# Performance work log

Hardware: AMD Instinct MI355X
Metric: run time of the kernel (lower is better)

Reference implementation:

```python
import jax, jax.numpy as jnp
import numpy as np

L = 262144      # number of points
C = 256         # in_channels
NH = 8          # num_heads
G = 64          # group_size
FF = 2048       # torch TransformerEncoderLayer default dim_feedforward
LPAD = 262144   # padded length, divisible by G; LPAD//G divisible by batch_size
BS = 4


def setup_inputs() -> dict:
    key = jax.random.key(0)
    ks = jax.random.split(key, 12)
    def w(k, shape, scale=0.02):
        return jax.random.normal(k, shape, jnp.float32) * scale
    return {
        "feats_flat": jax.random.normal(ks[0], (L, C), jnp.float32),
        "x_idx": jax.random.randint(ks[1], (L,), 0, L),
        "flat2win": jax.random.randint(ks[2], (LPAD,), 0, L),
        "win2flat": jax.random.randint(ks[3], (L,), 0, LPAD),
        "in_proj_w": w(ks[4], (3 * C, C)),
        "in_proj_b": jnp.zeros((3 * C,), jnp.float32),
        "out_proj_w": w(ks[5], (C, C)),
        "out_proj_b": jnp.zeros((C,), jnp.float32),
        "lin1_w": w(ks[6], (FF, C)),
        "lin1_b": jnp.zeros((FF,), jnp.float32),
        "lin2_w": w(ks[7], (C, FF)),
        "lin2_b": jnp.zeros((C,), jnp.float32),
        "ln1_g": jnp.ones((C,), jnp.float32),
        "ln1_b": jnp.zeros((C,), jnp.float32),
        "ln2_g": jnp.ones((C,), jnp.float32),
        "ln2_b": jnp.zeros((C,), jnp.float32),
        "proj_w": w(ks[8], (C, 2 * C)),
        "proj_b": jnp.zeros((C,), jnp.float32),
        "batch_size": BS,
    }


def _layer_norm(x, g, b, eps=1e-5):
    mu = jnp.mean(x, axis=-1, keepdims=True)
    var = jnp.var(x, axis=-1, keepdims=True)
    return (x - mu) * jax.lax.rsqrt(var + eps) * g + b


def _mha(x, in_proj_w, in_proj_b, out_proj_w, out_proj_b):
    B, S, Cm = x.shape
    hd = Cm // NH
    qkv = x @ in_proj_w.T + in_proj_b                      # [B,S,3C]
    q, k, v = jnp.split(qkv, 3, axis=-1)
    q = q.reshape(B, S, NH, hd)
    k = k.reshape(B, S, NH, hd)
    v = v.reshape(B, S, NH, hd)
    scores = jnp.einsum("bqhd,bkhd->bhqk", q, k) / jnp.sqrt(jnp.float32(hd))
    attn = jax.nn.softmax(scores, axis=-1)
    out = jnp.einsum("bhqk,bkhd->bqhd", attn, v).reshape(B, S, Cm)
    return out @ out_proj_w.T + out_proj_b


def reference(feats_flat, x_idx, flat2win, win2flat,
              in_proj_w, in_proj_b, out_proj_w, out_proj_b,
              lin1_w, lin1_b, lin2_w, lin2_b,
              ln1_g, ln1_b, ln2_g, ln2_b,
              proj_w, proj_b, batch_size):
    Cc = feats_flat.shape[1]
    # gather: feats_flat[indices][flat2win] -> [NW, G, C]
    feats_win = feats_flat[x_idx][flat2win].reshape(-1, G, Cc)
    # adaptive max pool over the group axis -> [NW, C]
    feats_pool = jnp.max(feats_win, axis=1)
    # torch TransformerEncoderLayer (post-norm, relu, eval/no-dropout)
    x = feats_pool.reshape(batch_size, -1, Cc)             # [B, S, C]
    x = _layer_norm(x + _mha(x, in_proj_w, in_proj_b, out_proj_w, out_proj_b), ln1_g, ln1_b)
    ff = jax.nn.relu(x @ lin1_w.T + lin1_b) @ lin2_w.T + lin2_b
    x = _layer_norm(x + ff, ln2_g, ln2_b)
    feats_global = x.reshape(-1, Cc)                       # [NW, C]
    # broadcast global feature to every group element, concat (global first)
    fuse_in = jnp.concatenate(
        [jnp.broadcast_to(feats_global[:, None, :], feats_win.shape), feats_win],
        axis=-1)                                           # [NW, G, 2C]
    feats_fuse = (fuse_in @ proj_w.T + proj_b).reshape(-1, Cc)  # [LPAD, C]
    # scatter back: feats_flat[indices] = feats_fuse[win2flat]
    return feats_flat.at[x_idx].set(feats_fuse[win2flat])
```

## Files before the change

### kernel.cpp

```cpp
#include <hip/hip_runtime.h>
#include <math.h>

namespace {
constexpr int kL    = 262144;
constexpr int kC    = 256;
constexpr int kNH   = 8;
constexpr int kG    = 64;
constexpr int kFF   = 2048;
constexpr int kLPAD = 262144;
constexpr int kBS   = 4;
constexpr int kNW   = kLPAD / kG;
constexpr int kS    = kNW / kBS;
constexpr int kHD   = kC / kNH;

constexpr size_t MB        = 1024 * 1024;
constexpr size_t OFF_GIDX   = 0;
constexpr size_t OFF_WINNER = 1 * MB;
constexpr size_t OFF_WLIST  = 2 * MB;
constexpr size_t OFF_CNT    = 3 * MB;
constexpr size_t OFF_X0     = 4 * MB;
constexpr size_t OFF_BASE   = 8 * MB;
constexpr size_t OFF_ATTN   = 12 * MB;
constexpr size_t OFF_QH     = 16 * MB;
constexpr size_t OFF_KH     = 18 * MB;
constexpr size_t OFF_VH     = 20 * MB;
constexpr size_t OFF_X1     = 24 * MB;
constexpr size_t OFF_FF1    = 32 * MB;
constexpr size_t OFF_WINB   = 64 * MB;
constexpr size_t OFF_WOUTB  = OFF_WINB  + 512 * 1024;
constexpr size_t OFF_W1B    = OFF_WOUTB + 256 * 1024;
constexpr size_t OFF_W2B    = OFF_W1B   + 1536 * 1024;
constexpr size_t OFF_WP1B   = OFF_W2B   + 1536 * 1024;
constexpr size_t OFF_WP2B   = OFF_WP1B  + 256 * 1024;

typedef __attribute__((ext_vector_type(8))) short bf16x8;
typedef __attribute__((ext_vector_type(4))) float f32x4;

__device__ inline unsigned short f2bf(float f) {
  union { float f; unsigned int u; } x; x.f = f;
  unsigned int r = x.u + 0x7fff + ((x.u >> 16) & 1);
  return (unsigned short)(r >> 16);
}
}

__global__ __launch_bounds__(256) void k_initw(int* __restrict__ winner,
                                               int* __restrict__ cnt) {
  int i = blockIdx.x * 256 + threadIdx.x;
  ((int4*)winner)[i] = make_int4(-1, -1, -1, -1);
  if (i == 0) cnt[0] = 0;
}

__global__ __launch_bounds__(256) void k_winner(const int* __restrict__ x_idx,
                                                int* __restrict__ winner) {
  int i0 = (blockIdx.x * 256 + threadIdx.x) * 4;
  int4 xi = *(const int4*)&x_idx[i0];
  atomicMax(&winner[xi.x], i0);
  atomicMax(&winner[xi.y], i0 + 1);
  atomicMax(&winner[xi.z], i0 + 2);
  atomicMax(&winner[xi.w], i0 + 3);
}

__global__ __launch_bounds__(256) void k_fc(const int* __restrict__ x_idx,
                                            const int* __restrict__ winner,
                                            int* __restrict__ wlist,
                                            int* __restrict__ cnt,
                                            const float* __restrict__ in_proj_w,
                                            const float* __restrict__ out_proj_w,
                                            const float* __restrict__ lin1_w,
                                            const float* __restrict__ lin2_w,
                                            const float* __restrict__ proj_w,
                                            unsigned short* __restrict__ WINB,
                                            unsigned short* __restrict__ WOUTB,
                                            unsigned short* __restrict__ W1B,
                                            unsigned short* __restrict__ W2B,
                                            unsigned short* __restrict__ WP1,
                                            unsigned short* __restrict__ WP2) {
  int blk = blockIdx.x, t = threadIdx.x;
  if (blk < 256) {
    int i0 = (blk * 256 + t) * 4;
    int4 xi = *(const int4*)&x_idx[i0];
    #pragma unroll
    for (int j = 0; j < 4; ++j) {
      int i = i0 + j;
      int xv = (j == 0) ? xi.x : (j == 1) ? xi.y : (j == 2) ? xi.z : xi.w;
      if (winner[xv] == i) {
        int p = atomicAdd(cnt, 1);
        wlist[p] = i;
      }
    }
    return;
  }
  int b2 = blk - 256;
  const float* src = nullptr; unsigned short* dst = nullptr; int i = 0;
  if (b2 < 192)       { src = in_proj_w;  dst = WINB;  i = b2 * 256 + t; }
  else if (b2 < 256)  { src = out_proj_w; dst = WOUTB; i = (b2 - 192) * 256 + t; }
  else if (b2 < 768)  { src = lin1_w;     dst = W1B;   i = (b2 - 256) * 256 + t; }
  else if (b2 < 1280) { src = lin2_w;     dst = W2B;   i = (b2 - 768) * 256 + t; }
  else {
    int c = b2 - 1280;
    WP1[c * kC + t] = f2bf(proj_w[(size_t)c * (2 * kC) + t]);
    WP2[c * kC + t] = f2bf(proj_w[(size_t)c * (2 * kC) + kC + t]);
    return;
  }
  float4 v = ((const float4*)src)[i];
  ushort4 b;
  b.x = f2bf(v.x); b.y = f2bf(v.y); b.z = f2bf(v.z); b.w = f2bf(v.w);
  ((ushort4*)dst)[i] = b;
}

__global__ __launch_bounds__(256) void k_pc(const float* __restrict__ feats,
                                            const int* __restrict__ x_idx,
                                            const int* __restrict__ flat2win,
                                            const int* __restrict__ winner,
                                            int* __restrict__ gidx,
                                            float* __restrict__ x0,
                                            float* __restrict__ out) {
  int blk = blockIdx.x, t = threadIdx.x;
  int w = t >> 6, lane = t & 63;
  if (blk < kNW) {
    __shared__ int rows[kG];
    __shared__ __align__(16) float mred[4][kC];
    if (t < kG) {
      int g = x_idx[flat2win[blk * kG + t]];
      rows[t] = g;
      gidx[blk * kG + t] = g;
    }
    __syncthreads();
    float4 mx = make_float4(-INFINITY, -INFINITY, -INFINITY, -INFINITY);
    #pragma unroll
    for (int i = 0; i < 16; ++i) {
      int r = rows[w * 16 + i];
      float4 v = *(const float4*)&feats[(size_t)r * kC + lane * 4];
      mx.x = fmaxf(mx.x, v.x); mx.y = fmaxf(mx.y, v.y);
      mx.z = fmaxf(mx.z, v.z); mx.w = fmaxf(mx.w, v.w);
    }
    *(float4*)&mred[w][lane * 4] = mx;
    __syncthreads();
    x0[blk * kC + t] = fmaxf(fmaxf(mred[0][t], mred[1][t]),
                             fmaxf(mred[2][t], mred[3][t]));
    return;
  }
  int cb = blk - kNW;
  #pragma unroll
  for (int i = 0; i < 2; ++i) {
    int row = cb * 8 + w * 2 + i;
    if (winner[row] < 0) {
      *(float4*)&out[(size_t)row * kC + lane * 4] =
          *(const float4*)&feats[(size_t)row * kC + lane * 4];
    }
  }
}

__global__ __launch_bounds__(256) void k_gemm_qkv(const float* __restrict__ A,
                                                  const unsigned short* __restrict__ Wb,
                                                  const float* __restrict__ bias,
                                                  unsigned short* __restrict__ Qh,
                                                  unsigned short* __restrict__ Kh,
                                                  unsigned short* __restrict__ Vh) {
  const float scale = 0.17677669529663687f;
  const int m0 = blockIdx.y * 64;
  const int sec = blockIdx.x;
  const int t = threadIdx.x;
  const int lane = t & 63, w = t >> 6;
  const int c0 = w * 64;
  const int kb = lane >> 4, lr = lane & 15;

  __shared__ __align__(16) unsigned short As[64 * 256];

  f32x4 acc[4][4] = {};
  #pragma unroll
  for (int i = 0; i < 16; ++i) {
    int row = i * 4 + w;
    float4 f4 = *(const float4*)&A[(size_t)(m0 + row) * kC + lane * 4];
    ushort4 b4;
    b4.x = f2bf(f4.x); b4.y = f2bf(f4.y); b4.z = f2bf(f4.z); b4.w = f2bf(f4.w);
    unsigned int off = (((unsigned)row * 512u) + (unsigned)lane * 8u) ^ (((unsigned)row & 7u) << 4);
    *(ushort4*)((char*)As + off) = b4;
  }
  __syncthreads();

  #pragma unroll
  for (int ks = 0; ks < 8; ++ks) {
    const int k0 = ks * 32;
    bf16x8 a[4], b[4];
    #pragma unroll
    for (int rt = 0; rt < 4; ++rt) {
      int row = rt * 16 + lr;
      unsigned int off = (((unsigned)row * 512u) + (unsigned)(k0 + kb * 8) * 2u) ^
                         (((unsigned)row & 7u) << 4);
      a[rt] = *(const bf16x8*)((const char*)As + off);
    }
    #pragma unroll
    for (int ct = 0; ct < 4; ++ct) {
      int c = sec * kC + c0 + ct * 16 + lr;
      b[ct] = *(const bf16x8*)&Wb[(size_t)c * kC + k0 + kb * 8];
    }
    #pragma unroll
    for (int rt = 0; rt < 4; ++rt)
      #pragma unroll
      for (int ct = 0; ct < 4; ++ct)
        acc[rt][ct] = __builtin_amdgcn_mfma_f32_16x16x32_bf16(a[rt], b[ct], acc[rt][ct], 0, 0, 0);
  }

  unsigned short* dstbuf = (sec == 0) ? Qh : (sec == 1) ? Kh : Vh;
  #pragma unroll
  for (int rt = 0; rt < 4; ++rt) {
    #pragma unroll
    for (int r = 0; r < 4; ++r) {
      int row = m0 + rt * 16 + kb * 4 + r;
      int bb = row >> 10, s = row & 1023;
      #pragma unroll
      for (int ct = 0; ct < 4; ++ct) {
        int c = c0 + ct * 16 + lr;
        float v = acc[rt][ct][r] + bias[sec * kC + c];
        if (sec == 0) v *= scale;
        int h = c >> 5, d = c & 31;
        dstbuf[(((size_t)(bb * kNH + h) * kS) + s) * kHD + d] = f2bf(v);
      }
    }
  }
}

__global__ __launch_bounds__(256) void k_attn(const unsigned short* __restrict__ Qh,
                                              const unsigned short* __restrict__ Kh,
                                              const unsigned short* __restrict__ Vh,
                                              unsigned short* __restrict__ attn_out) {
  const int q0 = blockIdx.x * 64;
  const int bh = blockIdx.y;
  const int b = bh >> 3, h = bh & 7;
  const int t = threadIdx.x;
  const int lane = t & 63, w = t >> 6;
  const int kb = lane >> 4, lr = lane & 15;

  __shared__ __align__(16) unsigned short Ks[128][40];
  __shared__ __align__(16) unsigned short VTs[32][136];
  __shared__ __align__(16) unsigned short Ps[4][16][136];

  bf16x8 aq = *(const bf16x8*)(Qh + (((size_t)bh * kS) + q0 + w * 16 + lr) * kHD + kb * 8);

  const unsigned short* kbase = Kh + (size_t)bh * kS * kHD;
  const unsigned short* vbase = Vh + (size_t)bh * kS * kHD;

  float m[4], l[4];
  f32x4 O[2] = {};
  #pragma unroll
  for (int r = 0; r < 4; ++r) { m[r] = -INFINITY; l[r] = 0.f; }

  for (int kt = 0; kt < kS / 128; ++kt) {
    {
      int key = t >> 1, d0 = (t & 1) * 16;
      size_t srow = ((size_t)(kt * 128 + key)) * kHD + d0;
      bf16x8 kv0 = *(const bf16x8*)(kbase + srow);
      bf16x8 kv1 = *(const bf16x8*)(kbase + srow + 8);
      *(bf16x8*)&Ks[key][d0] = kv0;
      *(bf16x8*)&Ks[key][d0 + 8] = kv1;
      bf16x8 vv0 = *(const bf16x8*)(vbase + srow);
      bf16x8 vv1 = *(const bf16x8*)(vbase + srow + 8);
      #pragma unroll
      for (int i = 0; i < 8; ++i) {
        VTs[d0 + i][key] = (unsigned short)vv0[i];
        VTs[d0 + 8 + i][key] = (unsigned short)vv1[i];
      }
    }
    __syncthreads();

    f32x4 S[8] = {};
    #pragma unroll
    for (int ct = 0; ct < 8; ++ct) {
      bf16x8 bk = *(const bf16x8*)&Ks[ct * 16 + lr][kb * 8];
      S[ct] = __builtin_amdgcn_mfma_f32_16x16x32_bf16(aq, bk, S[ct], 0, 0, 0);
    }

    float alpha[4];
    #pragma unroll
    for (int r = 0; r < 4; ++r) {
      float tmax = -INFINITY;
      #pragma unroll
      for (int ct = 0; ct < 8; ++ct) tmax = fmaxf(tmax, S[ct][r]);
      #pragma unroll
      for (int off = 8; off; off >>= 1) tmax = fmaxf(tmax, __shfl_xor(tmax, off, 16));
      float newm = fmaxf(m[r], tmax);
      alpha[r] = __expf(m[r] - newm);
      float ps = 0.f;
      #pragma unroll
      for (int ct = 0; ct < 8; ++ct) {
        float p = __expf(S[ct][r] - newm);
        ps += p;
        Ps[w][kb * 4 + r][ct * 16 + lr] = f2bf(p);
      }
      #pragma unroll
      for (int off = 8; off; off >>= 1) ps += __shfl_xor(ps, off, 16);
      l[r] = l[r] * alpha[r] + ps;
      m[r] = newm;
    }
    #pragma unroll
    for (int r = 0; r < 4; ++r) { O[0][r] *= alpha[r]; O[1][r] *= alpha[r]; }

    #pragma unroll
    for (int ks = 0; ks < 4; ++ks) {
      bf16x8 ap = *(const bf16x8*)&Ps[w][lr][ks * 32 + kb * 8];
      #pragma unroll
      for (int ct = 0; ct < 2; ++ct) {
        bf16x8 bv = *(const bf16x8*)&VTs[ct * 16 + lr][ks * 32 + kb * 8];
        O[ct] = __builtin_amdgcn_mfma_f32_16x16x32_bf16(ap, bv, O[ct], 0, 0, 0);
      }
    }
    __syncthreads();
  }

  #pragma unroll
  for (int ct = 0; ct < 2; ++ct) {
    #pragma unroll
    for (int r = 0; r < 4; ++r) {
      size_t row = (size_t)b * kS + q0 + w * 16 + kb * 4 + r;
      attn_out[row * kC + h * kHD + ct * 16 + lr] = f2bf(O[ct][r] / l[r]);
    }
  }
}

template <bool DO_BASE>
__global__ __launch_bounds__(256) void k_gemm_ln(const unsigned short* __restrict__ A,
                                                 int K,
                                                 const unsigned short* __restrict__ Wb,
                                                 const float* __restrict__ bias,
                                                 const float* __restrict__ R,
                                                 const float* __restrict__ g,
                                                 const float* __restrict__ bb,
                                                 float* __restrict__ Out,
                                                 const unsigned short* __restrict__ WbB,
                                                 const float* __restrict__ biasB) {
  const int m0 = blockIdx.x * 16;
  const int t = threadIdx.x;
  const int lane = t & 63, w = t >> 6;
  const int c0 = w * 64;
  const int kb = lane >> 4, lr = lane & 15;

  __shared__ __align__(16) unsigned short As[16 * 256];
  __shared__ __align__(16) unsigned short Xs[16 * 256];
  __shared__ float red[2][16][4];

  f32x4 acc[4] = {};
  for (int kc = 0; kc < K; kc += 256) {
    #pragma unroll
    for (int i = 0; i < 2; ++i) {
      int idx = i * 256 + t;
      int row = idx >> 5, seg = idx & 31;
      bf16x8 v = *(const bf16x8*)&A[(size_t)(m0 + row) * K + kc + seg * 8];
      unsigned int off = (((unsigned)row * 512u) + (unsigned)seg * 16u) ^ (((unsigned)row & 7u) << 4);
      *(bf16x8*)((char*)As + off) = v;
    }
    __syncthreads();

    #pragma unroll
    for (int ks = 0; ks < 8; ++ks) {
      const int k0 = ks * 32;
      unsigned int aoff = (((unsigned)lr * 512u) + (unsigned)(k0 + kb * 8) * 2u) ^
                          (((unsigned)lr & 7u) << 4);
      bf16x8 a = *(const bf16x8*)((const char*)As + aoff);
      #pragma unroll
      for (int ct = 0; ct < 4; ++ct) {
        bf16x8 b = *(const bf16x8*)&Wb[(size_t)(c0 + ct * 16 + lr) * K + kc + k0 + kb * 8];
        acc[ct] = __builtin_amdgcn_mfma_f32_16x16x32_bf16(a, b, acc[ct], 0, 0, 0);
      }
    }
    __syncthreads();
  }

  float v[4][4];
  float s[4], sq[4];
  #pragma unroll
  for (int r = 0; r < 4; ++r) { s[r] = 0.f; sq[r] = 0.f; }
  #pragma unroll
  for (int r = 0; r < 4; ++r) {
    int row = m0 + kb * 4 + r;
    #pragma unroll
    for (int ct = 0; ct < 4; ++ct) {
      int c = c0 + ct * 16 + lr;
      float x = acc[ct][r] + bias[c] + R[(size_t)row * kC + c];
      v[r][ct] = x;
      s[r] += x;
      sq[r] += x * x;
    }
  }
  #pragma unroll
  for (int r = 0; r < 4; ++r) {
    #pragma unroll
    for (int off = 8; off; off >>= 1) {
      s[r]  += __shfl_xor(s[r], off, 16);
      sq[r] += __shfl_xor(sq[r], off, 16);
    }
    if (lr == 0) { red[0][kb * 4 + r][w] = s[r]; red[1][kb * 4 + r][w] = sq[r]; }
  }
  __syncthreads();

  #pragma unroll
  for (int r = 0; r < 4; ++r) {
    int lrow = kb * 4 + r;
    float su = red[0][lrow][0] + red[0][lrow][1] + red[0][lrow][2] + red[0][lrow][3];
    float sg = red[1][lrow][0] + red[1][lrow][1] + red[1][lrow][2] + red[1][lrow][3];
    float mu = su * (1.0f / kC);
    float var = sg * (1.0f / kC) - mu * mu;
    float rs = rsqrtf(var + 1e-5f);
    #pragma unroll
    for (int ct = 0; ct < 4; ++ct) {
      int c = c0 + ct * 16 + lr;
      float yv = (v[r][ct] - mu) * rs * g[c] + bb[c];
      if (!DO_BASE) {
        Out[(size_t)(m0 + lrow) * kC + c] = yv;
      } else {
        unsigned int off = (((unsigned)lrow * 512u) + (unsigned)c * 2u) ^ (((unsigned)lrow & 7u) << 4);
        *(unsigned short*)((char*)Xs + off) = f2bf(yv);
      }
    }
  }

  if (DO_BASE) {
    __syncthreads();
    f32x4 acc2[4] = {};
    #pragma unroll
    for (int ks = 0; ks < 8; ++ks) {
      const int k0 = ks * 32;
      unsigned int aoff = (((unsigned)lr * 512u) + (unsigned)(k0 + kb * 8) * 2u) ^
                          (((unsigned)lr & 7u) << 4);
      bf16x8 a = *(const bf16x8*)((const char*)Xs + aoff);
      #pragma unroll
      for (int ct = 0; ct < 4; ++ct) {
        bf16x8 b = *(const bf16x8*)&WbB[(size_t)(c0 + ct * 16 + lr) * kC + k0 + kb * 8];
        acc2[ct] = __builtin_amdgcn_mfma_f32_16x16x32_bf16(a, b, acc2[ct], 0, 0, 0);
      }
    }
    #pragma unroll
    for (int r = 0; r < 4; ++r) {
      int row = m0 + kb * 4 + r;
      #pragma unroll
      for (int ct = 0; ct < 4; ++ct) {
        int c = c0 + ct * 16 + lr;
        Out[(size_t)row * kC + c] = acc2[ct][r] + biasB[c];
      }
    }
  }
}

__global__ __launch_bounds__(256) void k_gemm_ff1(const float* __restrict__ A,
                                                  const unsigned short* __restrict__ Wb,
                                                  const float* __restrict__ bias,
                                                  unsigned short* __restrict__ Cc) {
  const int m0 = blockIdx.y * 64;
  const int nb = blockIdx.x * 256;
  const int t = threadIdx.x;
  const int lane = t & 63, w = t >> 6;
  const int c0 = nb + w * 64;
  const int kb = lane >> 4, lr = lane & 15;

  __shared__ __align__(16) unsigned short As[64 * 256];

  f32x4 acc[4][4] = {};
  #pragma unroll
  for (int i = 0; i < 16; ++i) {
    int row = i * 4 + w;
    float4 f4 = *(const float4*)&A[(size_t)(m0 + row) * kC + lane * 4];
    ushort4 b4;
    b4.x = f2bf(f4.x); b4.y = f2bf(f4.y); b4.z = f2bf(f4.z); b4.w = f2bf(f4.w);
    unsigned int off = (((unsigned)row * 512u) + (unsigned)lane * 8u) ^ (((unsigned)row & 7u) << 4);
    *(ushort4*)((char*)As + off) = b4;
  }
  __syncthreads();

  #pragma unroll
  for (int ks = 0; ks < 8; ++ks) {
    const int k0 = ks * 32;
    bf16x8 a[4], b[4];
    #pragma unroll
    for (int rt = 0; rt < 4; ++rt) {
      int row = rt * 16 + lr;
      unsigned int off = (((unsigned)row * 512u) + (unsigned)(k0 + kb * 8) * 2u) ^
                         (((unsigned)row & 7u) << 4);
      a[rt] = *(const bf16x8*)((const char*)As + off);
    }
    #pragma unroll
    for (int ct = 0; ct < 4; ++ct) {
      int c = c0 + ct * 16 + lr;
      b[ct] = *(const bf16x8*)&Wb[(size_t)c * kC + k0 + kb * 8];
    }
    #pragma unroll
    for (int rt = 0; rt < 4; ++rt)
      #pragma unroll
      for (int ct = 0; ct < 4; ++ct)
        acc[rt][ct] = __builtin_amdgcn_mfma_f32_16x16x32_bf16(a[rt], b[ct], acc[rt][ct], 0, 0, 0);
  }

  #pragma unroll
  for (int rt = 0; rt < 4; ++rt) {
    #pragma unroll
    for (int r = 0; r < 4; ++r) {
      int row = m0 + rt * 16 + kb * 4 + r;
      #pragma unroll
      for (int ct = 0; ct < 4; ++ct) {
        int c = c0 + ct * 16 + lr;
        float vv = fmaxf(acc[rt][ct][r] + bias[c], 0.f);
        Cc[(size_t)row * kFF + c] = f2bf(vv);
      }
    }
  }
}

__global__ __launch_bounds__(256) void k_fuse(const float* __restrict__ feats,
                                              const int* __restrict__ gidx,
                                              const int* __restrict__ wlist,
                                              const int* __restrict__ cnt,
                                              const int* __restrict__ win2flat,
                                              const int* __restrict__ x_idx,
                                              const float* __restrict__ base,
                                              const unsigned short* __restrict__ W2B,
                                              float* __restrict__ out) {
  const int count = cnt[0];
  const int r0 = blockIdx.x * 64;
  if (r0 >= count) return;
  const int nr = min(64, count - r0);
  const int t = threadIdx.x;
  const int lane = t & 63, w = t >> 6;

  __shared__ __align__(16) unsigned short As[64 * 256];
  __shared__ int dstrow[64], wwin[64], srcrow[64];

  if (t < 64) {
    int rr = min(r0 + t, count - 1);
    int i = wlist[rr];
    int j = win2flat[i];
    srcrow[t] = gidx[j];
    wwin[t] = j >> 6;
    dstrow[t] = x_idx[i];
  }
  __syncthreads();

  for (int i = 0; i < 16; ++i) {
    int row = i * 4 + w;
    float4 f4 = *(const float4*)&feats[(size_t)srcrow[row] * kC + lane * 4];
    ushort4 b4;
    b4.x = f2bf(f4.x); b4.y = f2bf(f4.y); b4.z = f2bf(f4.z); b4.w = f2bf(f4.w);
    unsigned int off = (((unsigned)row * 512u) + (unsigned)lane * 8u) ^ (((unsigned)row & 7u) << 4);
    *(ushort4*)((char*)As + off) = b4;
  }
  __syncthreads();

  const int c0 = w * 64;
  const int kb = lane >> 4;
  const int lr = lane & 15;
  f32x4 acc[4][4] = {};
  for (int ks = 0; ks < 8; ++ks) {
    const int k0 = ks * 32;
    bf16x8 a[4], b[4];
    #pragma unroll
    for (int rt = 0; rt < 4; ++rt) {
      int row = rt * 16 + lr;
      unsigned int off = (((unsigned)row * 512u) + (unsigned)(k0 + kb * 8) * 2u) ^
                         (((unsigned)row & 7u) << 4);
      a[rt] = *(const bf16x8*)((const char*)As + off);
    }
    #pragma unroll
    for (int ct = 0; ct < 4; ++ct) {
      int c = c0 + ct * 16 + lr;
      b[ct] = *(const bf16x8*)&W2B[(size_t)c * kC + k0 + kb * 8];
    }
    #pragma unroll
    for (int rt = 0; rt < 4; ++rt)
      #pragma unroll
      for (int ct = 0; ct < 4; ++ct)
        acc[rt][ct] = __builtin_amdgcn_mfma_f32_16x16x32_bf16(a[rt], b[ct], acc[rt][ct], 0, 0, 0);
  }

  #pragma unroll
  for (int rt = 0; rt < 4; ++rt) {
    #pragma unroll
    for (int r = 0; r < 4; ++r) {
      int row = rt * 16 + kb * 4 + r;
      if (row < nr) {
        size_t orow = (size_t)dstrow[row] * kC;
        size_t brow = (size_t)wwin[row] * kC;
        #pragma unroll
        for (int ct = 0; ct < 4; ++ct) {
          int c = c0 + ct * 16 + lr;
          out[orow + c] = acc[rt][ct][r] + base[brow + c];
        }
      }
    }
  }
}

extern "C" void kernel_launch(void* const* d_in, const int* in_sizes, int n_in,
                              void* d_out, int out_size, void* d_ws, size_t ws_size,
                              hipStream_t stream) {
  const float* feats      = (const float*)d_in[0];
  const int*   x_idx      = (const int*)d_in[1];
  const int*   flat2win   = (const int*)d_in[2];
  const int*   win2flat   = (const int*)d_in[3];
  const float* in_proj_w  = (const float*)d_in[4];
  const float* in_proj_b  = (const float*)d_in[5];
  const float* out_proj_w = (const float*)d_in[6];
  const float* out_proj_b = (const float*)d_in[7];
  const float* lin1_w     = (const float*)d_in[8];
  const float* lin1_b     = (const float*)d_in[9];
  const float* lin2_w     = (const float*)d_in[10];
  const float* lin2_b     = (const float*)d_in[11];
  const float* ln1_g      = (const float*)d_in[12];
  const float* ln1_b      = (const float*)d_in[13];
  const float* ln2_g      = (const float*)d_in[14];
  const float* ln2_b      = (const float*)d_in[15];
  const float* proj_w     = (const float*)d_in[16];
  const float* proj_b     = (const float*)d_in[17];

  char* ws = (char*)d_ws;
  int*   gidx   = (int*)(ws + OFF_GIDX);
  int*   winner = (int*)(ws + OFF_WINNER);
  int*   wlist  = (int*)(ws + OFF_WLIST);
  int*   cnt    = (int*)(ws + OFF_CNT);
  float* x0     = (float*)(ws + OFF_X0);
  float* basep  = (float*)(ws + OFF_BASE);
  float* x1     = (float*)(ws + OFF_X1);
  unsigned short* attnb = (unsigned short*)(ws + OFF_ATTN);
  unsigned short* Qh    = (unsigned short*)(ws + OFF_QH);
  unsigned short* Kh    = (unsigned short*)(ws + OFF_KH);
  unsigned short* Vh    = (unsigned short*)(ws + OFF_VH);
  unsigned short* ff1b  = (unsigned short*)(ws + OFF_FF1);
  unsigned short* WINB  = (unsigned short*)(ws + OFF_WINB);
  unsigned short* WOUTB = (unsigned short*)(ws + OFF_WOUTB);
  unsigned short* W1B   = (unsigned short*)(ws + OFF_W1B);
  unsigned short* W2B   = (unsigned short*)(ws + OFF_W2B);
  unsigned short* WP1B  = (unsigned short*)(ws + OFF_WP1B);
  unsigned short* WP2B  = (unsigned short*)(ws + OFF_WP2B);
  float* out    = (float*)d_out;

  k_initw<<<kL / 1024, 256, 0, stream>>>(winner, cnt);
  k_winner<<<kL / 1024, 256, 0, stream>>>(x_idx, winner);
  k_fc<<<256 + 1536, 256, 0, stream>>>(x_idx, winner, wlist, cnt,
                                       in_proj_w, out_proj_w, lin1_w, lin2_w, proj_w,
                                       WINB, WOUTB, W1B, W2B, WP1B, WP2B);
  k_pc<<<kNW + kL / 8, 256, 0, stream>>>(feats, x_idx, flat2win, winner, gidx, x0, out);

  k_gemm_qkv<<<dim3(3, kNW / 64), 256, 0, stream>>>(x0, WINB, in_proj_b, Qh, Kh, Vh);
  k_attn<<<dim3(kS / 64, kBS * kNH), 256, 0, stream>>>(Qh, Kh, Vh, attnb);
  k_gemm_ln<false><<<kNW / 16, 256, 0, stream>>>(
      attnb, kC, WOUTB, out_proj_b, x0, ln1_g, ln1_b, x1, nullptr, nullptr);
  k_gemm_ff1<<<dim3(kFF / 256, kNW / 64), 256, 0, stream>>>(x1, W1B, lin1_b, ff1b);
  k_gemm_ln<true><<<kNW / 16, 256, 0, stream>>>(
      ff1b, kFF, W2B, lin2_b, x1, ln2_g, ln2_b, basep, WP1B, proj_b);
  k_fuse<<<kL / 64, 256, 0, stream>>>(feats, gidx, wlist, cnt, win2flat, x_idx,
                                      basep, WP2B, out);
}
```

Before: 378.4 us.

## Merge transformer-layer kernels into one cooperative persistent kernel with grid syncs

The five transformer-stage kernels (QKV GEMM, attention, out-proj+LN1, FF1, FF2+LN2) are refactored into device bodies using a shared smem buffer and run inside a single cooperative launch. The stages are separated by grid.sync instead of separate kernel launches, and each block loops over work units. This removes four launch gaps and tail drains, but the kernel caps occupancy at the largest smem user, limits the grid to at most 512 blocks, and adds grid-wide barrier cost. It falls back to separate launches if cooperative launch is unavailable.

```diff
diff --git a/kernel.cpp b/kernel.cpp
--- a/kernel.cpp
+++ b/kernel.cpp
@@ -1,5 +1,8 @@
 #include <hip/hip_runtime.h>
+#include <hip/hip_cooperative_groups.h>
 #include <math.h>
+
+namespace cg = cooperative_groups;
 
 namespace {
 constexpr int kL    = 262144;
@@ -151,21 +154,20 @@
   }
 }
 
-__global__ __launch_bounds__(256) void k_gemm_qkv(const float* __restrict__ A,
-                                                  const unsigned short* __restrict__ Wb,
-                                                  const float* __restrict__ bias,
-                                                  unsigned short* __restrict__ Qh,
-                                                  unsigned short* __restrict__ Kh,
-                                                  unsigned short* __restrict__ Vh) {
+__device__ __forceinline__ void qkv_body(int sec, int my, char* smem,
+                                         const float* __restrict__ A,
+                                         const unsigned short* __restrict__ Wb,
+                                         const float* __restrict__ bias,
+                                         unsigned short* __restrict__ Qh,
+                                         unsigned short* __restrict__ Kh,
+                                         unsigned short* __restrict__ Vh) {
   const float scale = 0.17677669529663687f;
-  const int m0 = blockIdx.y * 64;
-  const int sec = blockIdx.x;
+  const int m0 = my * 64;
   const int t = threadIdx.x;
   const int lane = t & 63, w = t >> 6;
   const int c0 = w * 64;
   const int kb = lane >> 4, lr = lane & 15;
-
-  __shared__ __align__(16) unsigned short As[64 * 256];
+  char* As = smem;
 
   f32x4 acc[4][4] = {};
   #pragma unroll
@@ -175,7 +177,7 @@
     ushort4 b4;
     b4.x = f2bf(f4.x); b4.y = f2bf(f4.y); b4.z = f2bf(f4.z); b4.w = f2bf(f4.w);
     unsigned int off = (((unsigned)row * 512u) + (unsigned)lane * 8u) ^ (((unsigned)row & 7u) << 4);
-    *(ushort4*)((char*)As + off) = b4;
+    *(ushort4*)(As + off) = b4;
   }
   __syncthreads();
 
@@ -188,7 +190,7 @@
       int row = rt * 16 + lr;
       unsigned int off = (((unsigned)row * 512u) + (unsigned)(k0 + kb * 8) * 2u) ^
                          (((unsigned)row & 7u) << 4);
-      a[rt] = *(const bf16x8*)((const char*)As + off);
+      a[rt] = *(const bf16x8*)(As + off);
     }
     #pragma unroll
     for (int ct = 0; ct < 4; ++ct) {
@@ -221,20 +223,20 @@
   }
 }
 
-__global__ __launch_bounds__(256) void k_attn(const unsigned short* __restrict__ Qh,
-                                              const unsigned short* __restrict__ Kh,
-                                              const unsigned short* __restrict__ Vh,
-                                              unsigned short* __restrict__ attn_out) {
-  const int q0 = blockIdx.x * 64;
-  const int bh = blockIdx.y;
+__device__ __forceinline__ void attn_body(int bxq, int bh, char* smem,
+                                          const unsigned short* __restrict__ Qh,
+                                          const unsigned short* __restrict__ Kh,
+                                          const unsigned short* __restrict__ Vh,
+                                          unsigned short* __restrict__ attn_out) {
+  const int q0 = bxq * 64;
   const int b = bh >> 3, h = bh & 7;
   const int t = threadIdx.x;
   const int lane = t & 63, w = t >> 6;
   const int kb = lane >> 4, lr = lane & 15;
 
-  __shared__ __align__(16) unsigned short Ks[128][40];
-  __shared__ __align__(16) unsigned short VTs[32][136];
-  __shared__ __align__(16) unsigned short Ps[4][16][136];
+  unsigned short (*Ks)[40]       = (unsigned short (*)[40])(smem);
+  unsigned short (*VTs)[136]     = (unsigned short (*)[136])(smem + 10240);
+  unsigned short (*Ps)[16][136]  = (unsigned short (*)[16][136])(smem + 18944);
 
   bf16x8 aq = *(const bf16x8*)(Qh + (((size_t)bh * kS) + q0 + w * 16 + lr) * kHD + kb * 8);
 
@@ -319,25 +321,26 @@
 }
 
 template <bool DO_BASE>
-__global__ __launch_bounds__(256) void k_gemm_ln(const unsigned short* __restrict__ A,
-                                                 int K,
-                                                 const unsigned short* __restrict__ Wb,
-                                                 const float* __restrict__ bias,
-                                                 const float* __restrict__ R,
-                                                 const float* __restrict__ g,
-                                                 const float* __restrict__ bb,
-                                                 float* __restrict__ Out,
-                                                 const unsigned short* __restrict__ WbB,
-                                                 const float* __restrict__ biasB) {
-  const int m0 = blockIdx.x * 16;
+__device__ __forceinline__ void gemm_ln_body(int bx, char* smem,
+                                             const unsigned short* __restrict__ A,
+                                             int K,
+                                             const unsigned short* __restrict__ Wb,
+                                             const float* __restrict__ bias,
+                                             const float* __restrict__ R,
+                                             const float* __restrict__ g,
+                                             const float* __restrict__ bb,
+                                             float* __restrict__ Out,
+                                             const unsigned short* __restrict__ WbB,
+                                             const float* __restrict__ biasB) {
+  const int m0 = bx * 16;
   const int t = threadIdx.x;
   const int lane = t & 63, w = t >> 6;
   const int c0 = w * 64;
   const int kb = lane >> 4, lr = lane & 15;
 
-  __shared__ __align__(16) unsigned short As[16 * 256];
-  __shared__ __align__(16) unsigned short Xs[16 * 256];
-  __shared__ float red[2][16][4];
+  char* As = smem;
+  char* Xs = smem + 8192;
+  float (*red)[16][4] = (float (*)[16][4])(smem + 16384);
 
   f32x4 acc[4] = {};
   for (int kc = 0; kc < K; kc += 256) {
@@ -347,7 +350,7 @@
       int row = idx >> 5, seg = idx & 31;
       bf16x8 v = *(const bf16x8*)&A[(size_t)(m0 + row) * K + kc + seg * 8];
       unsigned int off = (((unsigned)row * 512u) + (unsigned)seg * 16u) ^ (((unsigned)row & 7u) << 4);
-      *(bf16x8*)((char*)As + off) = v;
+      *(bf16x8*)(As + off) = v;
     }
     __syncthreads();
 
@@ -356,7 +359,7 @@
       const int k0 = ks * 32;
       unsigned int aoff = (((unsigned)lr * 512u) + (unsigned)(k0 + kb * 8) * 2u) ^
                           (((unsigned)lr & 7u) << 4);
-      bf16x8 a = *(const bf16x8*)((const char*)As + aoff);
+      bf16x8 a = *(const bf16x8*)(As + aoff);
       #pragma unroll
       for (int ct = 0; ct < 4; ++ct) {
         bf16x8 b = *(const bf16x8*)&Wb[(size_t)(c0 + ct * 16 + lr) * K + kc + k0 + kb * 8];
@@ -409,7 +412,7 @@
         Out[(size_t)(m0 + lrow) * kC + c] = yv;
       } else {
         unsigned int off = (((unsigned)lrow * 512u) + (unsigned)c * 2u) ^ (((unsigned)lrow & 7u) << 4);
-        *(unsigned short*)((char*)Xs + off) = f2bf(yv);
+        *(unsigned short*)(Xs + off) = f2bf(yv);
       }
     }
   }
@@ -422,7 +425,7 @@
       const int k0 = ks * 32;
       unsigned int aoff = (((unsigned)lr * 512u) + (unsigned)(k0 + kb * 8) * 2u) ^
                           (((unsigned)lr & 7u) << 4);
-      bf16x8 a = *(const bf16x8*)((const char*)Xs + aoff);
+      bf16x8 a = *(const bf16x8*)(Xs + aoff);
       #pragma unroll
       for (int ct = 0; ct < 4; ++ct) {
         bf16x8 b = *(const bf16x8*)&WbB[(size_t)(c0 + ct * 16 + lr) * kC + k0 + kb * 8];
@@ -441,18 +444,18 @@
   }
 }
 
-__global__ __launch_bounds__(256) void k_gemm_ff1(const float* __restrict__ A,
-                                                  const unsigned short* __restrict__ Wb,
-                                                  const float* __restrict__ bias,
-                                                  unsigned short* __restrict__ Cc) {
-  const int m0 = blockIdx.y * 64;
-  const int nb = blockIdx.x * 256;
+__device__ __forceinline__ void ff1_body(int nx, int my, char* smem,
+                                         const float* __restrict__ A,
+                                         const unsigned short* __restrict__ Wb,
+                                         const float* __restrict__ bias,
+                                         unsigned short* __restrict__ Cc) {
+  const int m0 = my * 64;
+  const int nb = nx * 256;
   const int t = threadIdx.x;
   const int lane = t & 63, w = t >> 6;
   const int c0 = nb + w * 64;
   const int kb = lane >> 4, lr = lane & 15;
-
-  __shared__ __align__(16) unsigned short As[64 * 256];
+  char* As = smem;
 
   f32x4 acc[4][4] = {};
   #pragma unroll
@@ -462,7 +465,7 @@
     ushort4 b4;
     b4.x = f2bf(f4.x); b4.y = f2bf(f4.y); b4.z = f2bf(f4.z); b4.w = f2bf(f4.w);
     unsigned int off = (((unsigned)row * 512u) + (unsigned)lane * 8u) ^ (((unsigned)row & 7u) << 4);
-    *(ushort4*)((char*)As + off) = b4;
+    *(ushort4*)(As + off) = b4;
   }
   __syncthreads();
 
@@ -475,7 +478,7 @@
       int row = rt * 16 + lr;
       unsigned int off = (((unsigned)row * 512u) + (unsigned)(k0 + kb * 8) * 2u) ^
                          (((unsigned)row & 7u) << 4);
-      a[rt] = *(const bf16x8*)((const char*)As + off);
+      a[rt] = *(const bf16x8*)(As + off);
     }
     #pragma unroll
     for (int ct = 0; ct < 4; ++ct) {
@@ -502,6 +505,75 @@
       }
     }
   }
+}
+
+struct FormerArgs {
+  const float* x0;
+  const unsigned short* WINB; const float* in_proj_b;
+  unsigned short* Qh; unsigned short* Kh; unsigned short* Vh;
+  unsigned short* attnb;
+  const unsigned short* WOUTB; const float* out_proj_b;
+  const float* ln1_g; const float* ln1_b; float* x1;
+  const unsigned short* W1B; const float* lin1_b; unsigned short* ff1b;
+  const unsigned short* W2B; const float* lin2_b;
+  const float* ln2_g; const float* ln2_b;
+  const unsigned short* WP1B; const float* proj_b; float* basep;
+};
+
+__global__ __launch_bounds__(256, 2) void k_former(FormerArgs a) {
+  __shared__ __align__(16) char smem[36864];
+  cg::grid_group grid = cg::this_grid();
+  const int gsz = gridDim.x;
+
+  for (int u = blockIdx.x; u < 192; u += gsz) {
+    qkv_body(u % 3, u / 3, smem, a.x0, a.WINB, a.in_proj_b, a.Qh, a.Kh, a.Vh);
+    __syncthreads();
+  }
+  grid.sync();
+  for (int u = blockIdx.x; u < 512; u += gsz) {
+    attn_body(u % 16, u / 16, smem, a.Qh, a.Kh, a.Vh, a.attnb);
+    __syncthreads();
+  }
+  grid.sync();
+  for (int u = blockIdx.x; u < 256; u += gsz) {
+    gemm_ln_body<false>(u, smem, a.attnb, kC, a.WOUTB, a.out_proj_b,
+                        a.x0, a.ln1_g, a.ln1_b, a.x1, nullptr, nullptr);
+    __syncthreads();
+  }
+  grid.sync();
+  for (int u = blockIdx.x; u < 512; u += gsz) {
+    ff1_body(u % 8, u / 8, smem, a.x1, a.W1B, a.lin1_b, a.ff1b);
+    __syncthreads();
+  }
+  grid.sync();
+  for (int u = blockIdx.x; u < 256; u += gsz) {
+    gemm_ln_body<true>(u, smem, a.ff1b, kFF, a.W2B, a.lin2_b,
+                       a.x1, a.ln2_g, a.ln2_b, a.basep, a.WP1B, a.proj_b);
+    __syncthreads();
+  }
+}
+
+__global__ __launch_bounds__(256) void k_qkv_sa(FormerArgs a) {
+  __shared__ __align__(16) char smem[32768];
+  qkv_body(blockIdx.x, blockIdx.y, smem, a.x0, a.WINB, a.in_proj_b, a.Qh, a.Kh, a.Vh);
+}
+__global__ __launch_bounds__(256) void k_attn_sa(FormerArgs a) {
+  __shared__ __align__(16) char smem[36352];
+  attn_body(blockIdx.x, blockIdx.y, smem, a.Qh, a.Kh, a.Vh, a.attnb);
+}
+__global__ __launch_bounds__(256) void k_ln1_sa(FormerArgs a) {
+  __shared__ __align__(16) char smem[16896];
+  gemm_ln_body<false>(blockIdx.x, smem, a.attnb, kC, a.WOUTB, a.out_proj_b,
+                      a.x0, a.ln1_g, a.ln1_b, a.x1, nullptr, nullptr);
+}
+__global__ __launch_bounds__(256) void k_ff1_sa(FormerArgs a) {
+  __shared__ __align__(16) char smem[32768];
+  ff1_body(blockIdx.x, blockIdx.y, smem, a.x1, a.W1B, a.lin1_b, a.ff1b);
+}
+__global__ __launch_bounds__(256) void k_ln2_sa(FormerArgs a) {
+  __shared__ __align__(16) char smem[16896];
+  gemm_ln_body<true>(blockIdx.x, smem, a.ff1b, kFF, a.W2B, a.lin2_b,
+                     a.x1, a.ln2_g, a.ln2_b, a.basep, a.WP1B, a.proj_b);
 }
 
 __global__ __launch_bounds__(256) void k_fuse(const float* __restrict__ feats,
@@ -637,13 +709,45 @@
                                        WINB, WOUTB, W1B, W2B, WP1B, WP2B);
   k_pc<<<kNW + kL / 8, 256, 0, stream>>>(feats, x_idx, flat2win, winner, gidx, x0, out);
 
-  k_gemm_qkv<<<dim3(3, kNW / 64), 256, 0, stream>>>(x0, WINB, in_proj_b, Qh, Kh, Vh);
-  k_attn<<<dim3(kS / 64, kBS * kNH), 256, 0, stream>>>(Qh, Kh, Vh, attnb);
-  k_gemm_ln<false><<<kNW / 16, 256, 0, stream>>>(
-      attnb, kC, WOUTB, out_proj_b, x0, ln1_g, ln1_b, x1, nullptr, nullptr);
-  k_gemm_ff1<<<dim3(kFF / 256, kNW / 64), 256, 0, stream>>>(x1, W1B, lin1_b, ff1b);
-  k_gemm_ln<true><<<kNW / 16, 256, 0, stream>>>(
-      ff1b, kFF, W2B, lin2_b, x1, ln2_g, ln2_b, basep, WP1B, proj_b);
+  FormerArgs fa;
+  fa.x0 = x0; fa.WINB = WINB; fa.in_proj_b = in_proj_b;
+  fa.Qh = Qh; fa.Kh = Kh; fa.Vh = Vh;
+  fa.attnb = attnb;
+  fa.WOUTB = WOUTB; fa.out_proj_b = out_proj_b;
+  fa.ln1_g = ln1_g; fa.ln1_b = ln1_b; fa.x1 = x1;
+  fa.W1B = W1B; fa.lin1_b = lin1_b; fa.ff1b = ff1b;
+  fa.W2B = W2B; fa.lin2_b = lin2_b;
+  fa.ln2_g = ln2_g; fa.ln2_b = ln2_b;
+  fa.WP1B = WP1B; fa.proj_b = proj_b; fa.basep = basep;
+
+  bool done = false;
+  int dev = 0;
+  (void)hipGetDevice(&dev);
+  int coopAttr = 0;
+  (void)hipDeviceGetAttribute(&coopAttr, hipDeviceAttributeCooperativeLaunch, dev);
+  if (coopAttr) {
+    int maxB = 0;
+    hipError_t oe = hipOccupancyMaxActiveBlocksPerMultiprocessor(
+        &maxB, (const void*)k_former, 256, 0);
+    int ncu = 0;
+    (void)hipDeviceGetAttribute(&ncu, hipDeviceAttributeMultiprocessorCount, dev);
+    if (oe == hipSuccess && maxB >= 1 && ncu >= 1) {
+      int grid = maxB * ncu;
+      if (grid > 512) grid = 512;
+      void* kargs[] = { (void*)&fa };
+      hipError_t le = hipLaunchCooperativeKernel((void*)k_former, dim3(grid), dim3(256),
+                                                 kargs, 0, stream);
+      done = (le == hipSuccess);
+    }
+  }
+  if (!done) {
+    k_qkv_sa<<<dim3(3, kNW / 64), 256, 0, stream>>>(fa);
+    k_attn_sa<<<dim3(kS / 64, kBS * kNH), 256, 0, stream>>>(fa);
+    k_ln1_sa<<<kNW / 16, 256, 0, stream>>>(fa);
+    k_ff1_sa<<<dim3(kFF / 256, kNW / 64), 256, 0, stream>>>(fa);
+    k_ln2_sa<<<kNW / 16, 256, 0, stream>>>(fa);
+  }
+
   k_fuse<<<kL / 64, 256, 0, stream>>>(feats, gidx, wlist, cnt, win2flat, x_idx,
                                       basep, WP2B, out);
 }
```

Measured after the change: 516.9 us. +36.6%, slower.
